# Performance work log

Hardware: AMD Instinct MI355X
Metric: run time of the kernel (lower is better)

## Reference

```python
import jax, jax.numpy as jnp
import numpy as np

NTR = 4
DTR = 0.0
DELTA = 3


def _get_edges(im, ntr, dtr):
    # im: [N, H, W] float
    N, H, W = im.shape
    d = DELTA
    im_b = jnp.ones((N, H + 2 * d, W + 2 * d), im.dtype).at[:, d:d + H, d:d + W].set(im)
    r = lambda a, s: jnp.roll(a, s, axis=(1, 2))
    diff_11 = r(im_b, (1, 1)) - im_b
    diff_nn11 = r(im_b, (-1, -1)) - im_b
    diff_01 = r(im_b, (0, 1)) - im_b
    diff_n01 = r(im_b, (0, -1)) - im_b
    diff_10 = r(im_b, (1, 0)) - im_b
    diff_n10 = r(im_b, (-1, 0)) - im_b
    diff_n11 = r(im_b, (-1, 1)) - im_b
    diff_1n1 = r(im_b, (1, -1)) - im_b
    gt = lambda a, b: (a > b).astype(jnp.int32)
    thr = lambda dd: jnp.abs(dd) * (jnp.abs(dd) > dtr).astype(im.dtype)

    ad_10 = thr(diff_10)
    c10 = (gt(ad_10, jnp.abs(diff_01)) + gt(ad_10, jnp.abs(diff_n01)) + gt(ad_10, jnp.abs(diff_n10))
           + gt(ad_10, jnp.abs(r(diff_01, (1, 0)))) + gt(ad_10, jnp.abs(r(diff_n01, (1, 0)))) + gt(ad_10, jnp.abs(r(diff_01, (1, 0)))))
    e10 = (c10 > ntr) & (diff_10 > 0)
    e10n = (c10 > ntr) & (diff_10 < 0)

    ad_01 = thr(diff_01)
    c01 = (gt(ad_01, jnp.abs(diff_10)) + gt(ad_01, jnp.abs(diff_n10)) + gt(ad_01, jnp.abs(diff_n01))
           + gt(ad_01, jnp.abs(r(diff_10, (0, 1)))) + gt(ad_01, jnp.abs(r(diff_n10, (0, 1)))) + gt(ad_01, jnp.abs(r(diff_01, (0, 1)))))
    e01 = (c01 > ntr) & (diff_01 > 0)
    e01n = (c01 > ntr) & (diff_01 < 0)

    ad_11 = thr(diff_11)
    c11 = (gt(ad_11, jnp.abs(diff_n11)) + gt(ad_11, jnp.abs(diff_1n1)) + gt(ad_11, jnp.abs(diff_nn11))
           + gt(ad_11, jnp.abs(r(diff_n11, (1, 1)))) + gt(ad_11, jnp.abs(r(diff_1n1, (1, 1)))) + gt(ad_11, jnp.abs(r(diff_11, (1, 1)))))
    e11 = (c11 > ntr) & (diff_11 > 0)
    e11n = (c11 > ntr) & (diff_11 < 0)

    ad_n11 = thr(diff_n11)
    cn11 = (gt(ad_n11, jnp.abs(diff_11)) + gt(ad_n11, jnp.abs(diff_1n1)) + gt(ad_n11, jnp.abs(diff_nn11))
            + gt(ad_n11, jnp.abs(r(diff_11, (-1, 1)))) + gt(ad_n11, jnp.abs(r(diff_n11, (-1, 1)))) + gt(ad_n11, jnp.abs(r(diff_n11, (-1, 1)))))
    en11 = (cn11 > ntr) & (diff_n11 > 0)
    en11n = (cn11 > ntr) & (diff_n11 < 0)

    f = lambda b: jnp.where(b, jnp.array(1, im.dtype), jnp.array(0, im.dtype))
    edges = jnp.zeros((N, 8, H, W), im.dtype)
    edges = edges.at[:, 0, 2:H, 0:W].set(f(e10[:, d + 2:d + H, d:d + W]))
    edges = edges.at[:, 1, 0:H - 2, 0:W].set(f(e10n[:, d:d + H - 2, d:d + W]))
    edges = edges.at[:, 2, 0:H, 2:W].set(f(e01[:, d:d + H, d + 2:d + W]))
    edges = edges.at[:, 3, 0:H, 0:W - 2].set(f(e01n[:, d:d + H, d:d + W - 2]))
    edges = edges.at[:, 4, 2:H, 2:W].set(f(e11[:, d + 2:d + H, d + 2:d + W]))
    edges = edges.at[:, 5, 0:H - 2, 0:W - 2].set(f(e11n[:, d:d + H - 2, d:d + W - 2]))
    edges = edges.at[:, 6, 0:H - 2, 2:W].set(f(en11[:, d:d + H - 2, d + 2:d + W]))
    edges = edges.at[:, 7, 2:H, 0:W - 2].set(f(en11n[:, d + 2:d + H, d:d + W - 2]))
    return edges


def setup_inputs() -> dict:
    key = jax.random.key(0)
    x = jax.random.normal(key, (16, 3, 512, 512), dtype=jnp.float32)
    return {"x": x}


def reference(x):
    B, C, H, W = x.shape
    # pre_edges concatenates per-channel get_edges along dim 1 -> [B, 8*C, H, W]
    im = x.reshape(B * C, H, W)
    edges = _get_edges(im, NTR, DTR)  # [B*C, 8, H, W]
    return edges.reshape(B, C * 8, H, W)
```

## Files before the change

kernel.cpp:

```cpp
#include <hip/hip_runtime.h>


#define IMG_H 512
#define IMG_W 512

typedef float float4v __attribute__((ext_vector_type(4)));

__device__ __forceinline__ void edge_core(
    float pcc, float pmm, float pm0, float pmp,
    float p0m, float p0p, float ppm, float pp0, float ppp,
    float p0mm, float pmm0, float pmmmm, float pppmm,
    float o[8])
{
    float d10   = pm0 - pcc;
    float dn10  = pp0 - pcc;
    float d01   = p0m - pcc;
    float dn01  = p0p - pcc;
    float d11   = pmm - pcc;
    float dnn11 = ppp - pcc;
    float dn11  = ppm - pcc;
    float d1n1  = pmp - pcc;

    float a10 = fabsf(d10),  an10  = fabsf(dn10);
    float a01 = fabsf(d01),  an01  = fabsf(dn01);
    float a11 = fabsf(d11),  ann11 = fabsf(dnn11);
    float an11 = fabsf(dn11), a1n1 = fabsf(d1n1);

    int c10 = (int)(a10 > a01) + (int)(a10 > an01) + (int)(a10 > an10)
            + 2 * (int)(a10 > fabsf(pmm - pm0))
            + (int)(a10 > fabsf(pmp - pm0));

    int c01 = (int)(a01 > a10) + (int)(a01 > an10) + (int)(a01 > an01)
            + (int)(a01 > fabsf(pmm - p0m))
            + (int)(a01 > fabsf(ppm - p0m))
            + (int)(a01 > fabsf(p0mm - p0m));

    int c11 = (int)(a11 > an11) + (int)(a11 > a1n1) + (int)(a11 > ann11)
            + (int)(a11 > fabsf(p0mm - pmm))
            + (int)(a11 > fabsf(pmm0 - pmm))
            + (int)(a11 > fabsf(pmmmm - pmm));

    int cn11 = (int)(an11 > a11) + (int)(an11 > a1n1) + (int)(an11 > ann11)
             + (int)(an11 > fabsf(p0mm - ppm))
             + 2 * (int)(an11 > fabsf(pppmm - ppm));

    o[0] = (c10 > 4 && d10 > 0.f) ? 1.f : 0.f;
    o[1] = (c10 > 4 && d10 < 0.f) ? 1.f : 0.f;
    o[2] = (c01 > 4 && d01 > 0.f) ? 1.f : 0.f;
    o[3] = (c01 > 4 && d01 < 0.f) ? 1.f : 0.f;
    o[4] = (c11 > 4 && d11 > 0.f) ? 1.f : 0.f;
    o[5] = (c11 > 4 && d11 < 0.f) ? 1.f : 0.f;
    o[6] = (cn11 > 4 && dn11 > 0.f) ? 1.f : 0.f;
    o[7] = (cn11 > 4 && dn11 < 0.f) ? 1.f : 0.f;
}

__global__ __launch_bounds__(256) void edge_kernel(const float* __restrict__ in,
                                                   float* __restrict__ out,
                                                   int nimg) {
    int idx = blockIdx.x * blockDim.x + threadIdx.x;
    int wq = idx & (IMG_W / 4 - 1);
    int h = (idx >> 7) & (IMG_H - 1);
    int n = idx >> 16;
    if (n >= nimg) return;
    int w0 = wq * 4;

    const float* img = in + (size_t)n * IMG_H * IMG_W;

    float4v ov[8];

    bool interior = (h >= 2) & (h <= IMG_H - 3) & (w0 >= 4) & (w0 <= IMG_W - 8);

    if (interior) {
        const float* rowm2 = img + (h - 2) * IMG_W + w0;
        const float* rowm1 = img + (h - 1) * IMG_W + w0;
        const float* row0  = img + h * IMG_W + w0;
        const float* rowp1 = img + (h + 1) * IMG_W + w0;
        const float* rowp2 = img + (h + 2) * IMG_W + w0;

        float rm2[6], rm1[6], r0[7], rp1[6], rp2[4];
#pragma unroll
        for (int j = 0; j < 6; ++j) rm2[j] = rowm2[j - 2];
#pragma unroll
        for (int j = 0; j < 6; ++j) rm1[j] = rowm1[j - 1];
#pragma unroll
        for (int j = 0; j < 7; ++j) r0[j]  = row0[j - 2];
#pragma unroll
        for (int j = 0; j < 6; ++j) rp1[j] = rowp1[j - 1];
#pragma unroll
        for (int j = 0; j < 4; ++j) rp2[j] = rowp2[j - 2];

#pragma unroll
        for (int i = 0; i < 4; ++i) {
            float o[8];
            edge_core(r0[i + 2],
                      rm1[i], rm1[i + 1], rm1[i + 2],
                      r0[i + 1], r0[i + 3],
                      rp1[i], rp1[i + 1], rp1[i + 2],
                      r0[i],
                      rm2[i + 2],
                      rm2[i],
                      rp2[i],
                      o);
#pragma unroll
            for (int k = 0; k < 8; ++k) ov[k][i] = o[k];
        }
    } else {
        auto ld = [&](int hh, int ww) -> float {
            bool ib = (hh >= 0) & (hh < IMG_H) & (ww >= 0) & (ww < IMG_W);
            int hc = min(max(hh, 0), IMG_H - 1);
            int wc = min(max(ww, 0), IMG_W - 1);
            float v = img[hc * IMG_W + wc];
            return ib ? v : 1.0f;
        };
#pragma unroll
        for (int i = 0; i < 4; ++i) {
            int w = w0 + i;
            float o[8];
            edge_core(ld(h, w),
                      ld(h - 1, w - 1), ld(h - 1, w), ld(h - 1, w + 1),
                      ld(h, w - 1), ld(h, w + 1),
                      ld(h + 1, w - 1), ld(h + 1, w), ld(h + 1, w + 1),
                      ld(h, w - 2),
                      ld(h - 2, w),
                      ld(h - 2, w - 2),
                      ld(h + 2, w - 2),
                      o);
            bool hge2 = h >= 2, hlt = h < IMG_H - 2;
            bool wge2 = w >= 2, wlt = w < IMG_W - 2;
            ov[0][i] = (hge2)         ? o[0] : 0.f;
            ov[1][i] = (hlt)          ? o[1] : 0.f;
            ov[2][i] = (wge2)         ? o[2] : 0.f;
            ov[3][i] = (wlt)          ? o[3] : 0.f;
            ov[4][i] = (hge2 && wge2) ? o[4] : 0.f;
            ov[5][i] = (hlt && wlt)   ? o[5] : 0.f;
            ov[6][i] = (hlt && wge2)  ? o[6] : 0.f;
            ov[7][i] = (hge2 && wlt)  ? o[7] : 0.f;
        }
    }

    const size_t cs = (size_t)IMG_H * IMG_W;
    float* obase = out + ((size_t)n * 8) * cs + (size_t)h * IMG_W + w0;
#pragma unroll
    for (int k = 0; k < 8; ++k) {
        __builtin_nontemporal_store(ov[k], (float4v*)(obase + (size_t)k * cs));
    }
}

extern "C" void kernel_launch(void* const* d_in, const int* in_sizes, int n_in,
                              void* d_out, int out_size, void* d_ws, size_t ws_size,
                              hipStream_t stream) {
    const float* x = (const float*)d_in[0];
    float* out = (float*)d_out;
    int nimg = in_sizes[0] / (IMG_H * IMG_W);
    long long total = (long long)nimg * IMG_H * (IMG_W / 4);
    int block = 256;
    int grid = (int)((total + block - 1) / block);
    edge_kernel<<<grid, block, 0, stream>>>(x, out, nimg);
}
```

Measured before the change: 82.95 us.

## Compute two output rows per thread and swizzle block order across XCDs

Each thread now produces a 2x4 output tile instead of 1x4. It loads six input rows once and reuses them for both rows, which cuts redundant global loads. Block indices are also remapped so consecutive logical blocks are spread across the 8 XCDs, improving L2 locality of neighbouring rows. The cost is higher register pressure, half as many threads, and a swizzle that assumes the grid size divides evenly by 8.

```diff
diff --git a/kernel.cpp b/kernel.cpp
--- a/kernel.cpp
+++ b/kernel.cpp
@@ -57,52 +57,87 @@
 __global__ __launch_bounds__(256) void edge_kernel(const float* __restrict__ in,
                                                    float* __restrict__ out,
                                                    int nimg) {
-    int idx = blockIdx.x * blockDim.x + threadIdx.x;
+    int bid = blockIdx.x;
+    int cpx = gridDim.x >> 3;
+    int swz = (bid & 7) * cpx + (bid >> 3);
+    int idx = swz * 256 + threadIdx.x;
+
     int wq = idx & (IMG_W / 4 - 1);
-    int h = (idx >> 7) & (IMG_H - 1);
-    int n = idx >> 16;
+    int hp = (idx >> 7) & (IMG_H / 2 - 1);
+    int n  = idx >> 15;
     if (n >= nimg) return;
     int w0 = wq * 4;
+    int h0 = hp * 2;
 
     const float* img = in + (size_t)n * IMG_H * IMG_W;
+    const size_t cs = (size_t)IMG_H * IMG_W;
+    float* obase = out + ((size_t)n * 8) * cs + (size_t)h0 * IMG_W + w0;
 
-    float4v ov[8];
-
-    bool interior = (h >= 2) & (h <= IMG_H - 3) & (w0 >= 4) & (w0 <= IMG_W - 8);
+    bool interior = (h0 >= 2) & (h0 <= IMG_H - 4) & (w0 >= 4) & (w0 <= IMG_W - 8);
 
     if (interior) {
-        const float* rowm2 = img + (h - 2) * IMG_W + w0;
-        const float* rowm1 = img + (h - 1) * IMG_W + w0;
-        const float* row0  = img + h * IMG_W + w0;
-        const float* rowp1 = img + (h + 1) * IMG_W + w0;
-        const float* rowp2 = img + (h + 2) * IMG_W + w0;
+        const float* rA = img + (h0 - 2) * IMG_W + w0 - 2;
+        const float* rB = img + (h0 - 1) * IMG_W + w0 - 2;
+        const float* rC = img + (h0    ) * IMG_W + w0 - 2;
+        const float* rD = img + (h0 + 1) * IMG_W + w0 - 2;
+        const float* rE = img + (h0 + 2) * IMG_W + w0 - 2;
+        const float* rF = img + (h0 + 3) * IMG_W + w0 - 2;
 
-        float rm2[6], rm1[6], r0[7], rp1[6], rp2[4];
+        float a[6], b[7], c[7], d[7], e[7], f[4];
 #pragma unroll
-        for (int j = 0; j < 6; ++j) rm2[j] = rowm2[j - 2];
+        for (int j = 0; j < 6; ++j) a[j] = rA[j];
 #pragma unroll
-        for (int j = 0; j < 6; ++j) rm1[j] = rowm1[j - 1];
+        for (int j = 0; j < 7; ++j) b[j] = rB[j];
 #pragma unroll
-        for (int j = 0; j < 7; ++j) r0[j]  = row0[j - 2];
+        for (int j = 0; j < 7; ++j) c[j] = rC[j];
 #pragma unroll
-        for (int j = 0; j < 6; ++j) rp1[j] = rowp1[j - 1];
+        for (int j = 0; j < 7; ++j) d[j] = rD[j];
 #pragma unroll
-        for (int j = 0; j < 4; ++j) rp2[j] = rowp2[j - 2];
+        for (int j = 0; j < 7; ++j) e[j] = rE[j];
+#pragma unroll
+        for (int j = 0; j < 4; ++j) f[j] = rF[j];
 
+        {
+            float4v ov[8];
 #pragma unroll
-        for (int i = 0; i < 4; ++i) {
-            float o[8];
-            edge_core(r0[i + 2],
-                      rm1[i], rm1[i + 1], rm1[i + 2],
-                      r0[i + 1], r0[i + 3],
-                      rp1[i], rp1[i + 1], rp1[i + 2],
-                      r0[i],
-                      rm2[i + 2],
-                      rm2[i],
-                      rp2[i],
-                      o);
+            for (int i = 0; i < 4; ++i) {
+                float o[8];
+                edge_core(c[i + 2],
+                          b[i + 1], b[i + 2], b[i + 3],
+                          c[i + 1], c[i + 3],
+                          d[i + 1], d[i + 2], d[i + 3],
+                          c[i],
+                          a[i + 2],
+                          a[i],
+                          e[i],
+                          o);
 #pragma unroll
-            for (int k = 0; k < 8; ++k) ov[k][i] = o[k];
+                for (int k = 0; k < 8; ++k) ov[k][i] = o[k];
+            }
+#pragma unroll
+            for (int k = 0; k < 8; ++k)
+                __builtin_nontemporal_store(ov[k], (float4v*)(obase + (size_t)k * cs));
+        }
+        {
+            float4v ov[8];
+#pragma unroll
+            for (int i = 0; i < 4; ++i) {
+                float o[8];
+                edge_core(d[i + 2],
+                          c[i + 1], c[i + 2], c[i + 3],
+                          d[i + 1], d[i + 3],
+                          e[i + 1], e[i + 2], e[i + 3],
+                          d[i],
+                          b[i + 2],
+                          b[i],
+                          f[i],
+                          o);
+#pragma unroll
+                for (int k = 0; k < 8; ++k) ov[k][i] = o[k];
+            }
+#pragma unroll
+            for (int k = 0; k < 8; ++k)
+                __builtin_nontemporal_store(ov[k], (float4v*)(obase + (size_t)k * cs + IMG_W));
         }
     } else {
         auto ld = [&](int hh, int ww) -> float {
@@ -113,36 +148,38 @@
             return ib ? v : 1.0f;
         };
 #pragma unroll
-        for (int i = 0; i < 4; ++i) {
-            int w = w0 + i;
-            float o[8];
-            edge_core(ld(h, w),
-                      ld(h - 1, w - 1), ld(h - 1, w), ld(h - 1, w + 1),
-                      ld(h, w - 1), ld(h, w + 1),
-                      ld(h + 1, w - 1), ld(h + 1, w), ld(h + 1, w + 1),
-                      ld(h, w - 2),
-                      ld(h - 2, w),
-                      ld(h - 2, w - 2),
-                      ld(h + 2, w - 2),
-                      o);
+        for (int r = 0; r < 2; ++r) {
+            int h = h0 + r;
             bool hge2 = h >= 2, hlt = h < IMG_H - 2;
-            bool wge2 = w >= 2, wlt = w < IMG_W - 2;
-            ov[0][i] = (hge2)         ? o[0] : 0.f;
-            ov[1][i] = (hlt)          ? o[1] : 0.f;
-            ov[2][i] = (wge2)         ? o[2] : 0.f;
-            ov[3][i] = (wlt)          ? o[3] : 0.f;
-            ov[4][i] = (hge2 && wge2) ? o[4] : 0.f;
-            ov[5][i] = (hlt && wlt)   ? o[5] : 0.f;
-            ov[6][i] = (hlt && wge2)  ? o[6] : 0.f;
-            ov[7][i] = (hge2 && wlt)  ? o[7] : 0.f;
+            float4v ov[8];
+#pragma unroll
+            for (int i = 0; i < 4; ++i) {
+                int w = w0 + i;
+                float o[8];
+                edge_core(ld(h, w),
+                          ld(h - 1, w - 1), ld(h - 1, w), ld(h - 1, w + 1),
+                          ld(h, w - 1), ld(h, w + 1),
+                          ld(h + 1, w - 1), ld(h + 1, w), ld(h + 1, w + 1),
+                          ld(h, w - 2),
+                          ld(h - 2, w),
+                          ld(h - 2, w - 2),
+                          ld(h + 2, w - 2),
+                          o);
+                bool wge2 = w >= 2, wlt = w < IMG_W - 2;
+                ov[0][i] = (hge2)         ? o[0] : 0.f;
+                ov[1][i] = (hlt)          ? o[1] : 0.f;
+                ov[2][i] = (wge2)         ? o[2] : 0.f;
+                ov[3][i] = (wlt)          ? o[3] : 0.f;
+                ov[4][i] = (hge2 && wge2) ? o[4] : 0.f;
+                ov[5][i] = (hlt && wlt)   ? o[5] : 0.f;
+                ov[6][i] = (hlt && wge2)  ? o[6] : 0.f;
+                ov[7][i] = (hge2 && wlt)  ? o[7] : 0.f;
+            }
+#pragma unroll
+            for (int k = 0; k < 8; ++k)
+                __builtin_nontemporal_store(
+                    ov[k], (float4v*)(obase + (size_t)k * cs + r * IMG_W));
         }
-    }
-
-    const size_t cs = (size_t)IMG_H * IMG_W;
-    float* obase = out + ((size_t)n * 8) * cs + (size_t)h * IMG_W + w0;
-#pragma unroll
-    for (int k = 0; k < 8; ++k) {
-        __builtin_nontemporal_store(ov[k], (float4v*)(obase + (size_t)k * cs));
     }
 }
 
@@ -152,7 +189,7 @@
     const float* x = (const float*)d_in[0];
     float* out = (float*)d_out;
     int nimg = in_sizes[0] / (IMG_H * IMG_W);
-    long long total = (long long)nimg * IMG_H * (IMG_W / 4);
+    long long total = (long long)nimg * (IMG_H / 2) * (IMG_W / 4);
     int block = 256;
     int grid = (int)((total + block - 1) / block);
     edge_kernel<<<grid, block, 0, stream>>>(x, out, nimg);
```

Measured after the change: 115.2 us. +38.9%, slower.
